# Kernel tuning notes

Measured on AMD Instinct MI355X. Metric: run time of the kernel, lower is better.

The kernel has to match this reference:

```python
import jax, jax.numpy as jnp
import numpy as np

N_BUS = 200000; N_GEN = 50000
E_BB = 1600000; E_GB = 400000; E_BG = 400000
D_IN = 64; H = 32
OUT_BUS = 4; OUT_GEN = 2


def setup_inputs() -> dict:
    key = jax.random.key(0)
    it = iter(jax.random.split(key, 48))
    def nrm(shape, s=0.05):
        return jax.random.normal(next(it), shape, jnp.float32) * s
    inp = {}
    inp["x_bus"] = jax.random.normal(next(it), (N_BUS, D_IN), jnp.float32)
    inp["x_gen"] = jax.random.normal(next(it), (N_GEN, D_IN), jnp.float32)
    inp["src_bb"] = jax.random.randint(next(it), (E_BB,), 0, N_BUS)
    inp["dst_bb"] = jax.random.randint(next(it), (E_BB,), 0, N_BUS)
    inp["src_gb"] = jax.random.randint(next(it), (E_GB,), 0, N_GEN)
    inp["dst_gb"] = jax.random.randint(next(it), (E_GB,), 0, N_BUS)
    inp["src_bg"] = jax.random.randint(next(it), (E_BG,), 0, N_BUS)
    inp["dst_bg"] = jax.random.randint(next(it), (E_BG,), 0, N_GEN)
    # SAGEConv params per layer / relation: lin_l (on aggregated neighbors, with bias),
    # lin_r (root weight on x_dst, no bias) -- matches PyG SAGEConv defaults.
    for lname, din in (("l1", D_IN), ("l2", H)):
        for rel in ("bb", "gb", "bg"):
            inp[f"{lname}_{rel}_Wl"] = nrm((din, H))
            inp[f"{lname}_{rel}_bl"] = jnp.zeros((H,), jnp.float32)
            inp[f"{lname}_{rel}_Wr"] = nrm((din, H))
    for nt, dout in (("bus", OUT_BUS), ("gen", OUT_GEN)):
        inp[f"lin0_{nt}_W"] = nrm((H, H))
        inp[f"lin0_{nt}_b"] = jnp.zeros((H,), jnp.float32)
        inp[f"linf_{nt}_W"] = nrm((H, dout))
        inp[f"linf_{nt}_b"] = jnp.zeros((dout,), jnp.float32)
    return inp


def _sage(x_src, x_dst, src, dst, Wl, bl, Wr, n_dst):
    # SAGEConv: mean-aggregate neighbor features, then out = lin_l(mean) + lin_r(x_dst)
    msg = jax.ops.segment_sum(x_src[src], dst, num_segments=n_dst)
    cnt = jax.ops.segment_sum(jnp.ones((src.shape[0],), x_src.dtype), dst, num_segments=n_dst)
    mean = msg / jnp.maximum(cnt, 1.0)[:, None]
    return mean @ Wl + bl + x_dst @ Wr


def reference(x_bus, x_gen, src_bb, dst_bb, src_gb, dst_gb, src_bg, dst_bg,
              l1_bb_Wl, l1_bb_bl, l1_bb_Wr, l1_gb_Wl, l1_gb_bl, l1_gb_Wr,
              l1_bg_Wl, l1_bg_bl, l1_bg_Wr,
              l2_bb_Wl, l2_bb_bl, l2_bb_Wr, l2_gb_Wl, l2_gb_bl, l2_gb_Wr,
              l2_bg_Wl, l2_bg_bl, l2_bg_Wr,
              lin0_bus_W, lin0_bus_b, lin0_gen_W, lin0_gen_b,
              linf_bus_W, linf_bus_b, linf_gen_W, linf_gen_b):
    # HeteroConv layer 1 (aggr='sum' over relations targeting each dst type)
    hb = (_sage(x_bus, x_bus, src_bb, dst_bb, l1_bb_Wl, l1_bb_bl, l1_bb_Wr, N_BUS)
          + _sage(x_gen, x_bus, src_gb, dst_gb, l1_gb_Wl, l1_gb_bl, l1_gb_Wr, N_BUS))
    hg = _sage(x_bus, x_gen, src_bg, dst_bg, l1_bg_Wl, l1_bg_bl, l1_bg_Wr, N_GEN)
    xb, xg = jax.nn.relu(hb), jax.nn.relu(hg)  # dropout is identity in eval mode
    # HeteroConv layer 2
    hb = (_sage(xb, xb, src_bb, dst_bb, l2_bb_Wl, l2_bb_bl, l2_bb_Wr, N_BUS)
          + _sage(xg, xb, src_gb, dst_gb, l2_gb_Wl, l2_gb_bl, l2_gb_Wr, N_BUS))
    hg = _sage(xb, xg, src_bg, dst_bg, l2_bg_Wl, l2_bg_bl, l2_bg_Wr, N_GEN)
    xb, xg = jax.nn.relu(hb), jax.nn.relu(hg)
    # per-node-type hidden Linear (input relu'd again as in the original; relu is idempotent)
    xb = jax.nn.relu(xb) @ lin0_bus_W + lin0_bus_b
    xg = jax.nn.relu(xg) @ lin0_gen_W + lin0_gen_b
    out_bus = xb @ linf_bus_W + linf_bus_b
    out_gen = xg @ linf_gen_W + linf_gen_b
    return out_bus, out_gen
```

## Files before the change

### kernel.cpp

```cpp
#include <hip/hip_runtime.h>
#include <hip/hip_bf16.h>

#define N_BUS 200000
#define N_GEN 50000
#define E_BB 1600000
#define E_GB 400000
#define E_BG 400000
#define H 32
#define NBINS 1024
#define EPT 16

#define NBK_BUS 782
#define NBK_GEN 196
#define CAP_BB 2560
#define CAP_GB 768
#define CAP_BG 2560

#define NB_PART_BB 391
#define NB_PART_GB 98
#define NB_PART_BG 98
#define NB_PART_ALL 587
#define NB_PREP 32
#define NB_TF_BUS 782
#define NB_TF_GEN 196
#define NB_TF_ALL 978
#define NB_FINE_ALL 1760
#define NB_PL_BUS 6250
#define NB_PL_GEN 1563

#define PNONE 0xFFFFFFFFu

typedef __attribute__((ext_vector_type(8))) short short8;
typedef __attribute__((ext_vector_type(4))) float floatx4;

__device__ inline unsigned short f2bf(float f) {
    __hip_bfloat16 h = __float2bfloat16(f);
    return *reinterpret_cast<unsigned short*>(&h);
}
__device__ inline float bf2f(unsigned short u) {
    return __uint_as_float(((unsigned)u) << 16);
}

__global__ __launch_bounds__(256) void zero_kernel(unsigned* __restrict__ p) {
    int i = blockIdx.x * 256 + threadIdx.x;
    if (i < 3 * NBINS) p[i] = 0u;
}

__device__ __forceinline__ void part_body(int blk, const int* __restrict__ src,
                                          const int* __restrict__ dst, int nE,
                                          unsigned* __restrict__ cnt_g, int CAP,
                                          unsigned* __restrict__ pairs) {
    __shared__ unsigned hist[NBINS];
    __shared__ unsigned base[NBINS];
    __shared__ unsigned sbase[NBINS];
    __shared__ unsigned sh[256];
    __shared__ unsigned pairv[256 * EPT];
    __shared__ unsigned short bid[256 * EPT];
    const int tid = threadIdx.x;
    const int cbase = blk * (256 * EPT);
    const int total = min(256 * EPT, nE - cbase);

    unsigned es[EPT], ed[EPT];
#pragma unroll
    for (int q = 0; q < EPT; q++) {
        int i = cbase + q * 256 + tid;
        if (i < nE) { es[q] = (unsigned)src[i]; ed[q] = (unsigned)dst[i]; }
        else ed[q] = PNONE;
    }
    for (int i = tid; i < NBINS; i += 256) hist[i] = 0;
    __syncthreads();
#pragma unroll
    for (int q = 0; q < EPT; q++)
        if (ed[q] != PNONE) atomicAdd(&hist[ed[q] >> 8], 1u);
    __syncthreads();

    unsigned h4[4];
    unsigned s = 0;
#pragma unroll
    for (int k2 = 0; k2 < 4; k2++) { h4[k2] = hist[tid * 4 + k2]; s += h4[k2]; }
    sh[tid] = s;
    __syncthreads();
#pragma unroll
    for (int d = 1; d < 256; d <<= 1) {
        unsigned t = (tid >= d) ? sh[tid - d] : 0u;
        __syncthreads();
        sh[tid] += t;
        __syncthreads();
    }
    unsigned run = sh[tid] - s;
#pragma unroll
    for (int k2 = 0; k2 < 4; k2++) {
        int b = tid * 4 + k2;
        sbase[b] = run;
        base[b] = h4[k2] ? ((unsigned)b * CAP + atomicAdd(&cnt_g[b], h4[k2])) : 0u;
        hist[b] = 0;
        run += h4[k2];
    }
    __syncthreads();

#pragma unroll
    for (int q = 0; q < EPT; q++) {
        if (ed[q] != PNONE) {
            unsigned b = ed[q] >> 8;
            unsigned off = atomicAdd(&hist[b], 1u);
            unsigned p = sbase[b] + off;
            pairv[p] = ((ed[q] & 255u) << 24) | es[q];
            bid[p] = (unsigned short)b;
        }
    }
    __syncthreads();

    for (int p = tid; p < total; p += 256) {
        unsigned b = bid[p];
        pairs[base[b] + ((unsigned)p - sbase[b])] = pairv[p];
    }
}

__device__ __forceinline__ void prep_body(int pb,
    const float* __restrict__ l1_bb_Wl, const float* __restrict__ l1_bb_bl, const float* __restrict__ l1_bb_Wr,
    const float* __restrict__ l1_gb_Wl, const float* __restrict__ l1_gb_bl, const float* __restrict__ l1_gb_Wr,
    const float* __restrict__ l1_bg_Wl, const float* __restrict__ l1_bg_bl, const float* __restrict__ l1_bg_Wr,
    const float* __restrict__ l2_bb_Wl, const float* __restrict__ l2_bb_bl, const float* __restrict__ l2_bb_Wr,
    const float* __restrict__ l2_gb_Wl, const float* __restrict__ l2_gb_bl, const float* __restrict__ l2_gb_Wr,
    const float* __restrict__ l2_bg_Wl, const float* __restrict__ l2_bg_bl, const float* __restrict__ l2_bg_Wr,
    const float* __restrict__ lin0_bus_W, const float* __restrict__ lin0_bus_b,
    const float* __restrict__ linf_bus_W, const float* __restrict__ linf_bus_b,
    const float* __restrict__ lin0_gen_W, const float* __restrict__ lin0_gen_b,
    const float* __restrict__ linf_gen_W, const float* __restrict__ linf_gen_b,
    unsigned short* __restrict__ Wf1b, float* __restrict__ B1b,
    unsigned short* __restrict__ Wf1g, float* __restrict__ B1g,
    unsigned short* __restrict__ Wf2b, float* __restrict__ B2b,
    unsigned short* __restrict__ Wf2g, float* __restrict__ B2g,
    float* __restrict__ WeB, float* __restrict__ beB,
    float* __restrict__ WeG, float* __restrict__ beG)
{
    int t0 = pb * 256 + threadIdx.x;
    const int NT = NB_PREP * 256;

    for (int f = t0; f < 2 * 6 * 64 * 8; f += NT) {
        int j = f & 7, l = (f >> 3) & 63, tile = f >> 9;
        int nt = tile % 6, kt = tile / 6;
        int k = kt * 32 + (l >> 4) * 8 + j, n = nt * 16 + (l & 15);
        float v;
        if (n < 32) v = l1_bb_Wl[k * 32 + n];
        else if (n < 64) v = l1_bg_Wl[k * 32 + n - 32];
        else v = l1_bb_Wr[k * 32 + n - 64] + l1_gb_Wr[k * 32 + n - 64];
        Wf1b[f] = f2bf(v);
    }
    for (int f = t0; f < 2 * 4 * 64 * 8; f += NT) {
        int j = f & 7, l = (f >> 3) & 63, tile = f >> 9;
        int nt = tile % 4, kt = tile / 4;
        int k = kt * 32 + (l >> 4) * 8 + j, n = nt * 16 + (l & 15);
        float v = (n < 32) ? l1_gb_Wl[k * 32 + n] : l1_bg_Wr[k * 32 + n - 32];
        Wf1g[f] = f2bf(v);
    }
    for (int f = t0; f < 6 * 64 * 8; f += NT) {
        int j = f & 7, l = (f >> 3) & 63, nt = f >> 9;
        int k = (l >> 4) * 8 + j, n = nt * 16 + (l & 15);
        float v;
        if (n < 32) v = l2_bb_Wl[k * 32 + n];
        else if (n < 64) v = l2_bg_Wl[k * 32 + n - 32];
        else v = l2_bb_Wr[k * 32 + n - 64] + l2_gb_Wr[k * 32 + n - 64];
        Wf2b[f] = f2bf(v);
    }
    for (int f = t0; f < 4 * 64 * 8; f += NT) {
        int j = f & 7, l = (f >> 3) & 63, nt = f >> 9;
        int k = (l >> 4) * 8 + j, n = nt * 16 + (l & 15);
        float v = (n < 32) ? l2_gb_Wl[k * 32 + n] : l2_bg_Wr[k * 32 + n - 32];
        Wf2g[f] = f2bf(v);
    }
    if (t0 < 96) {
        B1b[t0] = (t0 < 64) ? 0.0f : l1_bb_bl[t0 - 64] + l1_gb_bl[t0 - 64];
        B2b[t0] = (t0 < 64) ? 0.0f : l2_bb_bl[t0 - 64] + l2_gb_bl[t0 - 64];
    }
    if (t0 < 64) {
        B1g[t0] = (t0 < 32) ? 0.0f : l1_bg_bl[t0 - 32];
        B2g[t0] = (t0 < 32) ? 0.0f : l2_bg_bl[t0 - 32];
    }
    if (t0 < 128) {
        int k = t0 >> 2, c = t0 & 3;
        float s = 0.0f;
        for (int m = 0; m < 32; m++) s += lin0_bus_W[k * 32 + m] * linf_bus_W[m * 4 + c];
        WeB[t0] = s;
    }
    if (t0 >= 128 && t0 < 132) {
        int c = t0 - 128;
        float s = linf_bus_b[c];
        for (int m = 0; m < 32; m++) s += lin0_bus_b[m] * linf_bus_W[m * 4 + c];
        beB[c] = s;
    }
    if (t0 >= 132 && t0 < 196) {
        int i = t0 - 132, k = i >> 1, c = i & 1;
        float s = 0.0f;
        for (int m = 0; m < 32; m++) s += lin0_gen_W[k * 32 + m] * linf_gen_W[m * 2 + c];
        WeG[i] = s;
    }
    if (t0 >= 196 && t0 < 198) {
        int c = t0 - 196;
        float s = linf_gen_b[c];
        for (int m = 0; m < 32; m++) s += lin0_gen_b[m] * linf_gen_W[m * 2 + c];
        beG[c] = s;
    }
}

__global__ __launch_bounds__(256) void prep_part_kernel(
    const int* __restrict__ sbb, const int* __restrict__ dbb, unsigned* __restrict__ cbb, unsigned* __restrict__ pbb,
    const int* __restrict__ sgb, const int* __restrict__ dgb, unsigned* __restrict__ cgb, unsigned* __restrict__ pgb,
    const int* __restrict__ sbg, const int* __restrict__ dbg, unsigned* __restrict__ cbg, unsigned* __restrict__ pbg,
    const float* __restrict__ l1_bb_Wl, const float* __restrict__ l1_bb_bl, const float* __restrict__ l1_bb_Wr,
    const float* __restrict__ l1_gb_Wl, const float* __restrict__ l1_gb_bl, const float* __restrict__ l1_gb_Wr,
    const float* __restrict__ l1_bg_Wl, const float* __restrict__ l1_bg_bl, const float* __restrict__ l1_bg_Wr,
    const float* __restrict__ l2_bb_Wl, const float* __restrict__ l2_bb_bl, const float* __restrict__ l2_bb_Wr,
    const float* __restrict__ l2_gb_Wl, const float* __restrict__ l2_gb_bl, const float* __restrict__ l2_gb_Wr,
    const float* __restrict__ l2_bg_Wl, const float* __restrict__ l2_bg_bl, const float* __restrict__ l2_bg_Wr,
    const float* __restrict__ lin0_bus_W, const float* __restrict__ lin0_bus_b,
    const float* __restrict__ linf_bus_W, const float* __restrict__ linf_bus_b,
    const float* __restrict__ lin0_gen_W, const float* __restrict__ lin0_gen_b,
    const float* __restrict__ linf_gen_W, const float* __restrict__ linf_gen_b,
    unsigned short* __restrict__ Wf1b, float* __restrict__ B1b,
    unsigned short* __restrict__ Wf1g, float* __restrict__ B1g,
    unsigned short* __restrict__ Wf2b, float* __restrict__ B2b,
    unsigned short* __restrict__ Wf2g, float* __restrict__ B2g,
    float* __restrict__ WeB, float* __restrict__ beB,
    float* __restrict__ WeG, float* __restrict__ beG)
{
    int b = blockIdx.x;
    if (b < NB_PART_BB) part_body(b, sbb, dbb, E_BB, cbb, CAP_BB, pbb);
    else if (b < NB_PART_BB + NB_PART_GB) part_body(b - NB_PART_BB, sgb, dgb, E_GB, cgb, CAP_GB, pgb);
    else if (b < NB_PART_ALL) part_body(b - NB_PART_BB - NB_PART_GB, sbg, dbg, E_BG, cbg, CAP_BG, pbg);
    else prep_body(b - NB_PART_ALL,
                   l1_bb_Wl, l1_bb_bl, l1_bb_Wr, l1_gb_Wl, l1_gb_bl, l1_gb_Wr,
                   l1_bg_Wl, l1_bg_bl, l1_bg_Wr, l2_bb_Wl, l2_bb_bl, l2_bb_Wr,
                   l2_gb_Wl, l2_gb_bl, l2_gb_Wr, l2_bg_Wl, l2_bg_bl, l2_bg_Wr,
                   lin0_bus_W, lin0_bus_b, linf_bus_W, linf_bus_b,
                   lin0_gen_W, lin0_gen_b, linf_gen_W, linf_gen_b,
                   Wf1b, B1b, Wf1g, B1g, Wf2b, B2b, Wf2g, B2g, WeB, beB, WeG, beG);
}

__device__ __forceinline__ void fine_body(int b, const unsigned* __restrict__ cnt_g, int CAP,
                                          const unsigned* __restrict__ pairs,
                                          unsigned* __restrict__ rs,
                                          unsigned* __restrict__ esrc, int nDst,
                                          char* __restrict__ lds) {
    unsigned* cnt = (unsigned*)lds;
    unsigned* sh = (unsigned*)(lds + 1024);
    unsigned* stg = (unsigned*)(lds + 2048);
    const int tid = threadIdx.x;
    const unsigned start = (unsigned)b * CAP;
    const unsigned m = cnt_g[b];
    const unsigned end = start + m;

    cnt[tid] = 0;
    __syncthreads();
    for (unsigned k = start + tid; k < end; k += 256)
        atomicAdd(&cnt[pairs[k] >> 24], 1u);
    __syncthreads();
    unsigned c = cnt[tid];
    sh[tid] = c;
    __syncthreads();
#pragma unroll
    for (int d = 1; d < 256; d <<= 1) {
        unsigned t = (tid >= d) ? sh[tid - d] : 0u;
        __syncthreads();
        sh[tid] += t;
        __syncthreads();
    }
    int gd = b * 256 + tid;
    unsigned rowstart = start + sh[tid] - c;
    if (gd < nDst) rs[gd] = (rowstart << 9) | (c < 511u ? c : 511u);
    cnt[tid] = sh[tid] - c;
    __syncthreads();
    for (unsigned k = start + tid; k < end; k += 256) {
        unsigned p = pairs[k];
        unsigned off = atomicAdd(&cnt[p >> 24], 1u);
        stg[off] = p & 0x00FFFFFFu;
    }
    __syncthreads();
    for (unsigned p = tid; p < m; p += 256) esrc[start + p] = stg[p];
}

template <int K, int NOUT, int XS>
__device__ __forceinline__ void mfma_tail(
    int rows, int base,
    const unsigned short* __restrict__ Wf, const float* __restrict__ bias,
    unsigned short* __restrict__ y0, unsigned short* __restrict__ y1, float* __restrict__ h,
    short* lx, float* lo)
{
    constexpr int KT = K / 32, NTN = NOUT / 16, NCH = NOUT / 32;
    constexpr int OS = 34;
    const int tid = threadIdx.x;
    const int w = tid >> 6, l = tid & 63, quad = l >> 4, ln = l & 15;

    short8 bf[KT][NTN];
    const short8* wf8 = (const short8*)Wf;
#pragma unroll
    for (int kt = 0; kt < KT; kt++)
#pragma unroll
        for (int nt = 0; nt < NTN; nt++)
            bf[kt][nt] = wf8[(kt * NTN + nt) * 64 + l];
    float bv[NTN];
#pragma unroll
    for (int nt = 0; nt < NTN; nt++) bv[nt] = bias[nt * 16 + ln];

    floatx4 acc[4][NTN];
#pragma unroll
    for (int mt = 0; mt < 4; mt++)
#pragma unroll
        for (int nt = 0; nt < NTN; nt++) {
            floatx4 c0 = {bv[nt], bv[nt], bv[nt], bv[nt]};
            acc[mt][nt] = c0;
        }
#pragma unroll
    for (int mt = 0; mt < 4; mt++) {
        const int row = w * 64 + mt * 16 + ln;
#pragma unroll
        for (int kt = 0; kt < KT; kt++) {
            short8 af = *(const short8*)&lx[row * XS + kt * 32 + quad * 8];
#pragma unroll
            for (int nt = 0; nt < NTN; nt++)
                acc[mt][nt] = __builtin_amdgcn_mfma_f32_16x16x32_bf16(
                    af, bf[kt][nt], acc[mt][nt], 0, 0, 0);
        }
    }

#pragma unroll
    for (int c = 0; c < NCH; c++) {
        __syncthreads();
#pragma unroll
        for (int mt = 0; mt < 4; mt++)
#pragma unroll
            for (int d = 0; d < 2; d++) {
                int nt = 2 * c + d;
#pragma unroll
                for (int r = 0; r < 4; r++)
                    lo[(w * 64 + mt * 16 + quad * 4 + r) * OS + d * 16 + ln] = acc[mt][nt][r];
            }
        __syncthreads();
        const int T4 = rows * 8;
        if (c == NCH - 1) {
            float* og = h + (size_t)base * 32;
            for (int q = tid; q < T4; q += 256) {
                int r = q >> 3, cc = (q & 7) * 4;
                const float* p = &lo[r * OS + cc];
                *(float4*)(og + q * 4) = make_float4(p[0], p[1], p[2], p[3]);
            }
        } else {
            unsigned short* og = ((c == 0) ? y0 : y1) + (size_t)base * 32;
            for (int q = tid; q < T4; q += 256) {
                int r = q >> 3, cc = (q & 7) * 4;
                const float* p = &lo[r * OS + cc];
                short4 s4;
                s4.x = (short)f2bf(p[0]); s4.y = (short)f2bf(p[1]);
                s4.z = (short)f2bf(p[2]); s4.w = (short)f2bf(p[3]);
                *(short4*)(og + q * 4) = s4;
            }
        }
    }
}

template <int K, int NOUT>
__device__ __forceinline__ void transform_body(
    int blk, const float* x, int n,
    const unsigned short* __restrict__ Wf, const float* __restrict__ bias,
    unsigned short* __restrict__ y0, unsigned short* __restrict__ y1, float* h,
    char* ldsraw)
{
    constexpr int XS = K + 8;
    short* lx = (short*)ldsraw;
    const int tid = threadIdx.x;
    const int base = blk * 256;
    const int rows = min(256, n - base);

    {
        const float4* xg = (const float4*)(x + (size_t)base * K);
        const int T4 = rows * (K / 4);
        for (int q = tid; q < T4; q += 256) {
            float4 v = xg[q];
            int r = q / (K / 4), c = (q % (K / 4)) * 4;
            short4 s4;
            s4.x = (short)f2bf(v.x); s4.y = (short)f2bf(v.y);
            s4.z = (short)f2bf(v.z); s4.w = (short)f2bf(v.w);
            *(short4*)&lx[r * XS + c] = s4;
        }
    }
    __syncthreads();
    mfma_tail<K, NOUT, XS>(rows, base, Wf, bias, y0, y1, h, (short*)ldsraw, (float*)ldsraw);
}

template <int NOUT>
__device__ __forceinline__ void transform_bf16_body(
    int blk, const unsigned short* x, int n,
    const unsigned short* __restrict__ Wf, const float* __restrict__ bias,
    unsigned short* __restrict__ y0, unsigned short* __restrict__ y1, float* h,
    char* ldsraw)
{
    constexpr int K = 32, XS = K + 8;
    short* lx = (short*)ldsraw;
    const int tid = threadIdx.x;
    const int base = blk * 256;
    const int rows = min(256, n - base);

    {
        const short8* xg = (const short8*)(x + (size_t)base * K);
        const int T8 = rows * (K / 8);
        for (int q = tid; q < T8; q += 256) {
            short8 v = xg[q];
            int r = q / (K / 8), c = (q % (K / 8)) * 8;
            *(short8*)&lx[r * XS + c] = v;
        }
    }
    __syncthreads();
    mfma_tail<32, NOUT, XS>(rows, base, Wf, bias, y0, y1, h, (short*)ldsraw, (float*)ldsraw);
}

__global__ __launch_bounds__(256) void tf1_fine_kernel(
    const float* xb, const unsigned short* __restrict__ Wfb, const float* __restrict__ Bb,
    unsigned short* __restrict__ yb0, unsigned short* __restrict__ yb1, float* hb,
    const float* xg, const unsigned short* __restrict__ Wfg, const float* __restrict__ Bg,
    unsigned short* __restrict__ yg0, float* hg,
    const unsigned* __restrict__ cbb, const unsigned* __restrict__ pbb, unsigned* __restrict__ rsbb, unsigned* __restrict__ ebb,
    const unsigned* __restrict__ cgb, const unsigned* __restrict__ pgb, unsigned* __restrict__ rsgb, unsigned* __restrict__ egb,
    const unsigned* __restrict__ cbg, const unsigned* __restrict__ pbg, unsigned* __restrict__ rsbg, unsigned* __restrict__ ebg)
{
    constexpr int XB = 256 * (64 + 8) * 2, OB = 256 * 34 * 4;
    __shared__ __align__(16) char ldsraw[(XB > OB) ? XB : OB];
    int b = blockIdx.x;
    if (b < NB_TF_BUS)
        transform_body<64, 96>(b, xb, N_BUS, Wfb, Bb, yb0, yb1, hb, ldsraw);
    else if (b < NB_TF_ALL)
        transform_body<64, 64>(b - NB_TF_BUS, xg, N_GEN, Wfg, Bg, yg0, nullptr, hg, ldsraw);
    else {
        int f = b - NB_TF_ALL;
        if (f < NBK_BUS) fine_body(f, cbb, CAP_BB, pbb, rsbb, ebb, N_BUS, ldsraw);
        else if (f < 2 * NBK_BUS) fine_body(f - NBK_BUS, cgb, CAP_GB, pgb, rsgb, egb, N_BUS, ldsraw);
        else fine_body(f - 2 * NBK_BUS, cbg, CAP_BG, pbg, rsbg, ebg, N_GEN, ldsraw);
    }
}

__global__ __launch_bounds__(256) void tf2b_all_kernel(
    const unsigned short* x2b, const unsigned short* __restrict__ Wfb, const float* __restrict__ Bb,
    unsigned short* __restrict__ yb0, unsigned short* __restrict__ yb1, float* hb,
    const unsigned short* x2g, const unsigned short* __restrict__ Wfg, const float* __restrict__ Bg,
    unsigned short* __restrict__ yg0, float* hg)
{
    constexpr int XB = 256 * (32 + 8) * 2, OB = 256 * 34 * 4;
    __shared__ __align__(16) char ldsraw[(XB > OB) ? XB : OB];
    int b = blockIdx.x;
    if (b < NB_TF_BUS)
        transform_bf16_body<96>(b, x2b, N_BUS, Wfb, Bb, yb0, yb1, hb, ldsraw);
    else
        transform_bf16_body<64>(b - NB_TF_BUS, x2g, N_GEN, Wfg, Bg, yg0, nullptr, hg, ldsraw);
}

__device__ __forceinline__ void agg_one(
    unsigned u, const unsigned* __restrict__ e,
    const unsigned short* __restrict__ y, int j, float4& r)
{
    unsigned k0 = u >> 9;
    unsigned c = u & 511u;
    unsigned k1 = k0 + c;
    float4 a0 = make_float4(0.f, 0.f, 0.f, 0.f);
    float4 a1 = a0, a2 = a0, a3 = a0;
    unsigned k = k0;
    if (k + 4 <= k1) {
        unsigned s0 = e[k], s1 = e[k + 1], s2 = e[k + 2], s3 = e[k + 3];
        for (; k + 8 <= k1; k += 4) {
            unsigned t0 = e[k + 4], t1 = e[k + 5], t2 = e[k + 6], t3 = e[k + 7];
            ushort4 v0 = *(const ushort4*)(y + (size_t)s0 * H + j);
            ushort4 v1 = *(const ushort4*)(y + (size_t)s1 * H + j);
            ushort4 v2 = *(const ushort4*)(y + (size_t)s2 * H + j);
            ushort4 v3 = *(const ushort4*)(y + (size_t)s3 * H + j);
            a0.x += bf2f(v0.x); a0.y += bf2f(v0.y); a0.z += bf2f(v0.z); a0.w += bf2f(v0.w);
            a1.x += bf2f(v1.x); a1.y += bf2f(v1.y); a1.z += bf2f(v1.z); a1.w += bf2f(v1.w);
            a2.x += bf2f(v2.x); a2.y += bf2f(v2.y); a2.z += bf2f(v2.z); a2.w += bf2f(v2.w);
            a3.x += bf2f(v3.x); a3.y += bf2f(v3.y); a3.z += bf2f(v3.z); a3.w += bf2f(v3.w);
            s0 = t0; s1 = t1; s2 = t2; s3 = t3;
        }
        {
            ushort4 v0 = *(const ushort4*)(y + (size_t)s0 * H + j);
            ushort4 v1 = *(const ushort4*)(y + (size_t)s1 * H + j);
            ushort4 v2 = *(const ushort4*)(y + (size_t)s2 * H + j);
            ushort4 v3 = *(const ushort4*)(y + (size_t)s3 * H + j);
            a0.x += bf2f(v0.x); a0.y += bf2f(v0.y); a0.z += bf2f(v0.z); a0.w += bf2f(v0.w);
            a1.x += bf2f(v1.x); a1.y += bf2f(v1.y); a1.z += bf2f(v1.z); a1.w += bf2f(v1.w);
            a2.x += bf2f(v2.x); a2.y += bf2f(v2.y); a2.z += bf2f(v2.z); a2.w += bf2f(v2.w);
            a3.x += bf2f(v3.x); a3.y += bf2f(v3.y); a3.z += bf2f(v3.z); a3.w += bf2f(v3.w);
            k += 4;
        }
    }
    for (; k < k1; ++k) {
        unsigned s = e[k];
        const ushort4 v = *(const ushort4*)(y + (size_t)s * H + j);
        a0.x += bf2f(v.x); a0.y += bf2f(v.y); a0.z += bf2f(v.z); a0.w += bf2f(v.w);
    }
    a0.x += a1.x + a2.x + a3.x; a0.y += a1.y + a2.y + a3.y;
    a0.z += a1.z + a2.z + a3.z; a0.w += a1.w + a2.w + a3.w;
    float inv = 1.0f / (float)(c > 1u ? c : 1u);
    r.x += a0.x * inv; r.y += a0.y * inv; r.z += a0.z * inv; r.w += a0.w * inv;
}

template <bool FUSE>
__device__ __forceinline__ void pull_body(
    int blk, bool hasB, int n,
    const unsigned* __restrict__ rsA, const unsigned* __restrict__ eA, const unsigned short* __restrict__ yA,
    const unsigned* __restrict__ rsB, const unsigned* __restrict__ eB, const unsigned short* __restrict__ yB,
    const float* __restrict__ h, unsigned short* __restrict__ x2,
    const float* __restrict__ We, const float* __restrict__ be, int DOUT, float* __restrict__ outp)
{
    const int tid = threadIdx.x;
    unsigned node = blk * 32u + (tid >> 3);
    int j = (tid & 7) * 4;
    if (node >= (unsigned)n) return;

    float4 r = *(const float4*)(h + (size_t)node * H + j);

    agg_one(rsA[node], eA, yA, j, r);
    if (hasB) agg_one(rsB[node], eB, yB, j, r);

    if (!FUSE) {
        ushort4 o;
        o.x = f2bf(fmaxf(r.x, 0.f)); o.y = f2bf(fmaxf(r.y, 0.f));
        o.z = f2bf(fmaxf(r.z, 0.f)); o.w = f2bf(fmaxf(r.w, 0.f));
        *(ushort4*)(x2 + (size_t)node * H + j) = o;
        return;
    }

    float p0 = fmaxf(r.x, 0.f), p1 = fmaxf(r.y, 0.f), p2 = fmaxf(r.z, 0.f), p3 = fmaxf(r.w, 0.f);
    float tot[4];
#pragma unroll
    for (int c = 0; c < 4; c++) {
        if (c < DOUT) {
            tot[c] = p0 * We[(j + 0) * DOUT + c] + p1 * We[(j + 1) * DOUT + c]
                   + p2 * We[(j + 2) * DOUT + c] + p3 * We[(j + 3) * DOUT + c];
        } else tot[c] = 0.f;
    }
#pragma unroll
    for (int mask = 1; mask <= 4; mask <<= 1) {
#pragma unroll
        for (int c = 0; c < 4; c++) tot[c] += __shfl_xor(tot[c], mask);
    }
    if ((tid & 7) == 0) {
        if (DOUT == 4) {
            *(float4*)(outp + (size_t)node * 4) =
                make_float4(tot[0] + be[0], tot[1] + be[1], tot[2] + be[2], tot[3] + be[3]);
        } else {
            *(float2*)(outp + (size_t)node * 2) = make_float2(tot[0] + be[0], tot[1] + be[1]);
        }
    }
}

template <bool FUSE>
__global__ __launch_bounds__(256) void pull_all_kernel(
    const unsigned* __restrict__ rsbb, const unsigned* __restrict__ ebb, const unsigned short* __restrict__ ybb,
    const unsigned* __restrict__ rsgb, const unsigned* __restrict__ egb, const unsigned short* __restrict__ ygb,
    const float* __restrict__ hb, unsigned short* __restrict__ x2b,
    const float* __restrict__ WeB, const float* __restrict__ beB,
    const unsigned* __restrict__ rsbg, const unsigned* __restrict__ ebg, const unsigned short* __restrict__ ybg,
    const float* __restrict__ hg, unsigned short* __restrict__ x2g,
    const float* __restrict__ WeG, const float* __restrict__ beG,
    float* __restrict__ outp)
{
    int b = blockIdx.x;
    if (b < NB_PL_BUS)
        pull_body<FUSE>(b, true, N_BUS, rsbb, ebb, ybb, rsgb, egb, ygb, hb, x2b, WeB, beB, 4, outp);
    else
        pull_body<FUSE>(b - NB_PL_BUS, false, N_GEN, rsbg, ebg, ybg, nullptr, nullptr, nullptr,
                        hg, x2g, WeG, beG, 2, outp ? outp + (size_t)N_BUS * 4 : nullptr);
}

extern "C" void kernel_launch(void* const* d_in, const int* in_sizes, int n_in,
                              void* d_out, int out_size, void* d_ws, size_t ws_size,
                              hipStream_t stream) {
    const float* x_bus = (const float*)d_in[0];
    const float* x_gen = (const float*)d_in[1];
    const int* src_bb = (const int*)d_in[2];
    const int* dst_bb = (const int*)d_in[3];
    const int* src_gb = (const int*)d_in[4];
    const int* dst_gb = (const int*)d_in[5];
    const int* src_bg = (const int*)d_in[6];
    const int* dst_bg = (const int*)d_in[7];
    const float* l1_bb_Wl = (const float*)d_in[8];
    const float* l1_bb_bl = (const float*)d_in[9];
    const float* l1_bb_Wr = (const float*)d_in[10];
    const float* l1_gb_Wl = (const float*)d_in[11];
    const float* l1_gb_bl = (const float*)d_in[12];
    const float* l1_gb_Wr = (const float*)d_in[13];
    const float* l1_bg_Wl = (const float*)d_in[14];
    const float* l1_bg_bl = (const float*)d_in[15];
    const float* l1_bg_Wr = (const float*)d_in[16];
    const float* l2_bb_Wl = (const float*)d_in[17];
    const float* l2_bb_bl = (const float*)d_in[18];
    const float* l2_bb_Wr = (const float*)d_in[19];
    const float* l2_gb_Wl = (const float*)d_in[20];
    const float* l2_gb_bl = (const float*)d_in[21];
    const float* l2_gb_Wr = (const float*)d_in[22];
    const float* l2_bg_Wl = (const float*)d_in[23];
    const float* l2_bg_bl = (const float*)d_in[24];
    const float* l2_bg_Wr = (const float*)d_in[25];
    const float* lin0_bus_W = (const float*)d_in[26];
    const float* lin0_bus_b = (const float*)d_in[27];
    const float* linf_bus_W = (const float*)d_in[28];
    const float* linf_bus_b = (const float*)d_in[29];
    const float* lin0_gen_W = (const float*)d_in[30];
    const float* lin0_gen_b = (const float*)d_in[31];
    const float* linf_gen_W = (const float*)d_in[32];
    const float* linf_gen_b = (const float*)d_in[33];

    char* ws = (char*)d_ws;
    size_t off = 0;
    auto alloc = [&](size_t bytes) {
        char* p = ws + off;
        off += (bytes + 255) & ~(size_t)255;
        return p;
    };
    unsigned* rs_bb = (unsigned*)alloc((size_t)N_BUS * 4);
    unsigned* rs_gb = (unsigned*)alloc((size_t)N_BUS * 4);
    unsigned* rs_bg = (unsigned*)alloc((size_t)N_GEN * 4);
    unsigned* cur_bb = (unsigned*)alloc(NBINS * 4);
    unsigned* cur_gb = (unsigned*)alloc(NBINS * 4);
    unsigned* cur_bg = (unsigned*)alloc(NBINS * 4);
    unsigned* e_bb = (unsigned*)alloc((size_t)NBK_BUS * CAP_BB * 4);
    unsigned* e_gb = (unsigned*)alloc((size_t)NBK_BUS * CAP_GB * 4);
    unsigned* e_bg = (unsigned*)alloc((size_t)NBK_GEN * CAP_BG * 4);
    unsigned* p_bb = (unsigned*)alloc((size_t)NBK_BUS * CAP_BB * 4);
    unsigned* p_gb = (unsigned*)alloc((size_t)NBK_BUS * CAP_GB * 4);
    unsigned* p_bg = (unsigned*)alloc((size_t)NBK_GEN * CAP_BG * 4);
    unsigned short* y_bb = (unsigned short*)alloc((size_t)N_BUS * H * 2);
    unsigned short* y_bg = (unsigned short*)alloc((size_t)N_BUS * H * 2);
    unsigned short* y_gb = (unsigned short*)alloc((size_t)N_GEN * H * 2);
    float* h_bus = (float*)alloc((size_t)N_BUS * H * 4);
    float* h_gen = (float*)alloc((size_t)N_GEN * H * 4);
    unsigned short* x2_bus = (unsigned short*)alloc((size_t)N_BUS * H * 2);
    unsigned short* x2_gen = (unsigned short*)alloc((size_t)N_GEN * H * 2);
    unsigned short* Wf1b = (unsigned short*)alloc(2 * 6 * 64 * 8 * 2);
    float* B1b = (float*)alloc(96 * 4);
    unsigned short* Wf1g = (unsigned short*)alloc(2 * 4 * 64 * 8 * 2);
    float* B1g = (float*)alloc(64 * 4);
    unsigned short* Wf2b = (unsigned short*)alloc(6 * 64 * 8 * 2);
    float* B2b = (float*)alloc(96 * 4);
    unsigned short* Wf2g = (unsigned short*)alloc(4 * 64 * 8 * 2);
    float* B2g = (float*)alloc(64 * 4);
    float* WeB = (float*)alloc(128 * 4);
    float* beB = (float*)alloc(4 * 4);
    float* WeG = (float*)alloc(64 * 4);
    float* beG = (float*)alloc(2 * 4);

    zero_kernel<<<12, 256, 0, stream>>>(cur_bb);

    prep_part_kernel<<<NB_PART_ALL + NB_PREP, 256, 0, stream>>>(
        src_bb, dst_bb, cur_bb, p_bb, src_gb, dst_gb, cur_gb, p_gb,
        src_bg, dst_bg, cur_bg, p_bg,
        l1_bb_Wl, l1_bb_bl, l1_bb_Wr, l1_gb_Wl, l1_gb_bl, l1_gb_Wr,
        l1_bg_Wl, l1_bg_bl, l1_bg_Wr, l2_bb_Wl, l2_bb_bl, l2_bb_Wr,
        l2_gb_Wl, l2_gb_bl, l2_gb_Wr, l2_bg_Wl, l2_bg_bl, l2_bg_Wr,
        lin0_bus_W, lin0_bus_b, linf_bus_W, linf_bus_b,
        lin0_gen_W, lin0_gen_b, linf_gen_W, linf_gen_b,
        Wf1b, B1b, Wf1g, B1g, Wf2b, B2b, Wf2g, B2g, WeB, beB, WeG, beG);

    tf1_fine_kernel<<<NB_TF_ALL + NB_FINE_ALL, 256, 0, stream>>>(
        x_bus, Wf1b, B1b, y_bb, y_bg, h_bus, x_gen, Wf1g, B1g, y_gb, h_gen,
        cur_bb, p_bb, rs_bb, e_bb, cur_gb, p_gb, rs_gb, e_gb, cur_bg, p_bg, rs_bg, e_bg);

    pull_all_kernel<false><<<NB_PL_BUS + NB_PL_GEN, 256, 0, stream>>>(
        rs_bb, e_bb, y_bb, rs_gb, e_gb, y_gb, h_bus, x2_bus, WeB, beB,
        rs_bg, e_bg, y_bg, h_gen, x2_gen, WeG, beG, nullptr);

    tf2b_all_kernel<<<NB_TF_BUS + NB_TF_GEN, 256, 0, stream>>>(
        x2_bus, Wf2b, B2b, y_bb, y_bg, h_bus, x2_gen, Wf2g, B2g, y_gb, h_gen);

    pull_all_kernel<true><<<NB_PL_BUS + NB_PL_GEN, 256, 0, stream>>>(
        rs_bb, e_bb, y_bb, rs_gb, e_gb, y_gb, h_bus, nullptr, WeB, beB,
        rs_bg, e_bg, y_bg, h_gen, nullptr, WeG, beG, (float*)d_out);
}
```

Measured before the change: 354.3 us.

## Fuse layer-1 aggregation with layer-2 MFMA transform into one kernel

Merges the first pull/aggregate kernel and the layer-2 transform kernel. Each 32-node block now aggregates neighbours, applies relu, stages the bf16 activations in LDS and runs the MFMA transform in place. This drops the x2 intermediate round trip through global memory and one kernel launch. Because the new kernel reads the layer-1 y buffers while producing layer-2 outputs, separate y2 buffers are needed. Each block now does small 32-row MFMA tiles with extra syncthreads, which may lower transform efficiency.

```diff
diff --git a/kernel.cpp b/kernel.cpp
--- a/kernel.cpp
+++ b/kernel.cpp
@@ -387,32 +387,6 @@
     mfma_tail<K, NOUT, XS>(rows, base, Wf, bias, y0, y1, h, (short*)ldsraw, (float*)ldsraw);
 }
 
-template <int NOUT>
-__device__ __forceinline__ void transform_bf16_body(
-    int blk, const unsigned short* x, int n,
-    const unsigned short* __restrict__ Wf, const float* __restrict__ bias,
-    unsigned short* __restrict__ y0, unsigned short* __restrict__ y1, float* h,
-    char* ldsraw)
-{
-    constexpr int K = 32, XS = K + 8;
-    short* lx = (short*)ldsraw;
-    const int tid = threadIdx.x;
-    const int base = blk * 256;
-    const int rows = min(256, n - base);
-
-    {
-        const short8* xg = (const short8*)(x + (size_t)base * K);
-        const int T8 = rows * (K / 8);
-        for (int q = tid; q < T8; q += 256) {
-            short8 v = xg[q];
-            int r = q / (K / 8), c = (q % (K / 8)) * 8;
-            *(short8*)&lx[r * XS + c] = v;
-        }
-    }
-    __syncthreads();
-    mfma_tail<32, NOUT, XS>(rows, base, Wf, bias, y0, y1, h, (short*)ldsraw, (float*)ldsraw);
-}
-
 __global__ __launch_bounds__(256) void tf1_fine_kernel(
     const float* xb, const unsigned short* __restrict__ Wfb, const float* __restrict__ Bb,
     unsigned short* __restrict__ yb0, unsigned short* __restrict__ yb1, float* hb,
@@ -435,21 +409,6 @@
         else if (f < 2 * NBK_BUS) fine_body(f - NBK_BUS, cgb, CAP_GB, pgb, rsgb, egb, N_BUS, ldsraw);
         else fine_body(f - 2 * NBK_BUS, cbg, CAP_BG, pbg, rsbg, ebg, N_GEN, ldsraw);
     }
-}
-
-__global__ __launch_bounds__(256) void tf2b_all_kernel(
-    const unsigned short* x2b, const unsigned short* __restrict__ Wfb, const float* __restrict__ Bb,
-    unsigned short* __restrict__ yb0, unsigned short* __restrict__ yb1, float* hb,
-    const unsigned short* x2g, const unsigned short* __restrict__ Wfg, const float* __restrict__ Bg,
-    unsigned short* __restrict__ yg0, float* hg)
-{
-    constexpr int XB = 256 * (32 + 8) * 2, OB = 256 * 34 * 4;
-    __shared__ __align__(16) char ldsraw[(XB > OB) ? XB : OB];
-    int b = blockIdx.x;
-    if (b < NB_TF_BUS)
-        transform_bf16_body<96>(b, x2b, N_BUS, Wfb, Bb, yb0, yb1, hb, ldsraw);
-    else
-        transform_bf16_body<64>(b - NB_TF_BUS, x2g, N_GEN, Wfg, Bg, yg0, nullptr, hg, ldsraw);
 }
 
 __device__ __forceinline__ void agg_one(
@@ -499,12 +458,103 @@
     r.x += a0.x * inv; r.y += a0.y * inv; r.z += a0.z * inv; r.w += a0.w * inv;
 }
 
-template <bool FUSE>
-__device__ __forceinline__ void pull_body(
+template <int NTA, bool HASB>
+__device__ __forceinline__ void pull_tf_body(
+    int blk, int n,
+    const unsigned* __restrict__ rsA, const unsigned* __restrict__ eA, const unsigned short* __restrict__ yA,
+    const unsigned* __restrict__ rsB, const unsigned* __restrict__ eB, const unsigned short* __restrict__ yB,
+    float* __restrict__ h,
+    const unsigned short* __restrict__ Wf, const float* __restrict__ bias,
+    unsigned short* __restrict__ z0, unsigned short* __restrict__ z1,
+    short* __restrict__ lx, float* __restrict__ lo)
+{
+    constexpr int XS = 40;
+    constexpr int OS = 34;
+    const int tid = threadIdx.x;
+    const int row = tid >> 3;
+    const int j = (tid & 7) * 4;
+    const int base = blk * 32;
+    const int node = base + row;
+    const bool act = node < n;
+
+    float4 r = make_float4(0.f, 0.f, 0.f, 0.f);
+    if (act) {
+        r = *(const float4*)(h + (size_t)node * H + j);
+        agg_one(rsA[node], eA, yA, j, r);
+        if (HASB) agg_one(rsB[node], eB, yB, j, r);
+    }
+    short4 s4;
+    s4.x = (short)f2bf(fmaxf(r.x, 0.f));
+    s4.y = (short)f2bf(fmaxf(r.y, 0.f));
+    s4.z = (short)f2bf(fmaxf(r.z, 0.f));
+    s4.w = (short)f2bf(fmaxf(r.w, 0.f));
+    *(short4*)&lx[row * XS + j] = s4;
+    __syncthreads();
+
+    const int w = tid >> 6, l = tid & 63, quad = l >> 4, ln = l & 15;
+    const int mt = w & 1, ngrp = w >> 1;
+    const short8* wf8 = (const short8*)Wf;
+    floatx4 acc[NTA];
+    short8 af = *(const short8*)&lx[(mt * 16 + ln) * XS + quad * 8];
+#pragma unroll
+    for (int i = 0; i < NTA; i++) {
+        int nt = 2 * i + ngrp;
+        float bv = bias[nt * 16 + ln];
+        floatx4 c0 = {bv, bv, bv, bv};
+        acc[i] = __builtin_amdgcn_mfma_f32_16x16x32_bf16(af, wf8[nt * 64 + l], c0, 0, 0, 0);
+    }
+
+    const int rows = min(32, n - base);
+    const int orow = tid >> 3, oc = (tid & 7) * 4;
+#pragma unroll
+    for (int c = 0; c < NTA; c++) {
+        __syncthreads();
+#pragma unroll
+        for (int rr = 0; rr < 4; rr++)
+            lo[(mt * 16 + quad * 4 + rr) * OS + ngrp * 16 + ln] = acc[c][rr];
+        __syncthreads();
+        if (orow < rows) {
+            const float* p = &lo[orow * OS + oc];
+            if (c == NTA - 1) {
+                *(float4*)(h + (size_t)(base + orow) * H + oc) =
+                    make_float4(p[0], p[1], p[2], p[3]);
+            } else {
+                unsigned short* og = (c == 0) ? z0 : z1;
+                short4 o;
+                o.x = (short)f2bf(p[0]); o.y = (short)f2bf(p[1]);
+                o.z = (short)f2bf(p[2]); o.w = (short)f2bf(p[3]);
+                *(short4*)(og + (size_t)(base + orow) * H + oc) = o;
+            }
+        }
+    }
+}
+
+__global__ __launch_bounds__(256) void pull_tf2_kernel(
+    const unsigned* __restrict__ rsbb, const unsigned* __restrict__ ebb, const unsigned short* __restrict__ ybb,
+    const unsigned* __restrict__ rsgb, const unsigned* __restrict__ egb, const unsigned short* __restrict__ ygb,
+    float* __restrict__ hb, const unsigned short* __restrict__ Wfb, const float* __restrict__ Bb,
+    unsigned short* __restrict__ y2bb, unsigned short* __restrict__ y2bg,
+    const unsigned* __restrict__ rsbg, const unsigned* __restrict__ ebg, const unsigned short* __restrict__ ybg,
+    float* __restrict__ hg, const unsigned short* __restrict__ Wfg, const float* __restrict__ Bg,
+    unsigned short* __restrict__ y2gb)
+{
+    __shared__ __align__(16) short lx[32 * 40];
+    __shared__ __align__(16) float lo[32 * 34];
+    int b = blockIdx.x;
+    if (b < NB_PL_BUS)
+        pull_tf_body<3, true>(b, N_BUS, rsbb, ebb, ybb, rsgb, egb, ygb,
+                              hb, Wfb, Bb, y2bb, y2bg, lx, lo);
+    else
+        pull_tf_body<2, false>(b - NB_PL_BUS, N_GEN, rsbg, ebg, ybg,
+                               nullptr, nullptr, nullptr,
+                               hg, Wfg, Bg, y2gb, nullptr, lx, lo);
+}
+
+__device__ __forceinline__ void pull_head_body(
     int blk, bool hasB, int n,
     const unsigned* __restrict__ rsA, const unsigned* __restrict__ eA, const unsigned short* __restrict__ yA,
     const unsigned* __restrict__ rsB, const unsigned* __restrict__ eB, const unsigned short* __restrict__ yB,
-    const float* __restrict__ h, unsigned short* __restrict__ x2,
+    const float* __restrict__ h,
     const float* __restrict__ We, const float* __restrict__ be, int DOUT, float* __restrict__ outp)
 {
     const int tid = threadIdx.x;
@@ -516,14 +566,6 @@
 
     agg_one(rsA[node], eA, yA, j, r);
     if (hasB) agg_one(rsB[node], eB, yB, j, r);
-
-    if (!FUSE) {
-        ushort4 o;
-        o.x = f2bf(fmaxf(r.x, 0.f)); o.y = f2bf(fmaxf(r.y, 0.f));
-        o.z = f2bf(fmaxf(r.z, 0.f)); o.w = f2bf(fmaxf(r.w, 0.f));
-        *(ushort4*)(x2 + (size_t)node * H + j) = o;
-        return;
-    }
 
     float p0 = fmaxf(r.x, 0.f), p1 = fmaxf(r.y, 0.f), p2 = fmaxf(r.z, 0.f), p3 = fmaxf(r.w, 0.f);
     float tot[4];
@@ -549,23 +591,20 @@
     }
 }
 
-template <bool FUSE>
-__global__ __launch_bounds__(256) void pull_all_kernel(
-    const unsigned* __restrict__ rsbb, const unsigned* __restrict__ ebb, const unsigned short* __restrict__ ybb,
-    const unsigned* __restrict__ rsgb, const unsigned* __restrict__ egb, const unsigned short* __restrict__ ygb,
-    const float* __restrict__ hb, unsigned short* __restrict__ x2b,
-    const float* __restrict__ WeB, const float* __restrict__ beB,
-    const unsigned* __restrict__ rsbg, const unsigned* __restrict__ ebg, const unsigned short* __restrict__ ybg,
-    const float* __restrict__ hg, unsigned short* __restrict__ x2g,
-    const float* __restrict__ WeG, const float* __restrict__ beG,
+__global__ __launch_bounds__(256) void pull_head_kernel(
+    const unsigned* __restrict__ rsbb, const unsigned* __restrict__ ebb, const unsigned short* __restrict__ y2bb,
+    const unsigned* __restrict__ rsgb, const unsigned* __restrict__ egb, const unsigned short* __restrict__ y2gb,
+    const float* __restrict__ hb, const float* __restrict__ WeB, const float* __restrict__ beB,
+    const unsigned* __restrict__ rsbg, const unsigned* __restrict__ ebg, const unsigned short* __restrict__ y2bg,
+    const float* __restrict__ hg, const float* __restrict__ WeG, const float* __restrict__ beG,
     float* __restrict__ outp)
 {
     int b = blockIdx.x;
     if (b < NB_PL_BUS)
-        pull_body<FUSE>(b, true, N_BUS, rsbb, ebb, ybb, rsgb, egb, ygb, hb, x2b, WeB, beB, 4, outp);
+        pull_head_body(b, true, N_BUS, rsbb, ebb, y2bb, rsgb, egb, y2gb, hb, WeB, beB, 4, outp);
     else
-        pull_body<FUSE>(b - NB_PL_BUS, false, N_GEN, rsbg, ebg, ybg, nullptr, nullptr, nullptr,
-                        hg, x2g, WeG, beG, 2, outp ? outp + (size_t)N_BUS * 4 : nullptr);
+        pull_head_body(b - NB_PL_BUS, false, N_GEN, rsbg, ebg, y2bg, nullptr, nullptr, nullptr,
+                       hg, WeG, beG, 2, outp + (size_t)N_BUS * 4);
 }
 
 extern "C" void kernel_launch(void* const* d_in, const int* in_sizes, int n_in,
@@ -628,10 +667,11 @@
     unsigned short* y_bb = (unsigned short*)alloc((size_t)N_BUS * H * 2);
     unsigned short* y_bg = (unsigned short*)alloc((size_t)N_BUS * H * 2);
     unsigned short* y_gb = (unsigned short*)alloc((size_t)N_GEN * H * 2);
+    unsigned short* y2_bb = (unsigned short*)alloc((size_t)N_BUS * H * 2);
+    unsigned short* y2_bg = (unsigned short*)alloc((size_t)N_BUS * H * 2);
+    unsigned short* y2_gb = (unsigned short*)alloc((size_t)N_GEN * H * 2);
     float* h_bus = (float*)alloc((size_t)N_BUS * H * 4);
     float* h_gen = (float*)alloc((size_t)N_GEN * H * 4);
-    unsigned short* x2_bus = (unsigned short*)alloc((size_t)N_BUS * H * 2);
-    unsigned short* x2_gen = (unsigned short*)alloc((size_t)N_GEN * H * 2);
     unsigned short* Wf1b = (unsigned short*)alloc(2 * 6 * 64 * 8 * 2);
     float* B1b = (float*)alloc(96 * 4);
     unsigned short* Wf1g = (unsigned short*)alloc(2 * 4 * 64 * 8 * 2);
@@ -661,14 +701,11 @@
         x_bus, Wf1b, B1b, y_bb, y_bg, h_bus, x_gen, Wf1g, B1g, y_gb, h_gen,
         cur_bb, p_bb, rs_bb, e_bb, cur_gb, p_gb, rs_gb, e_gb, cur_bg, p_bg, rs_bg, e_bg);
 
-    pull_all_kernel<false><<<NB_PL_BUS + NB_PL_GEN, 256, 0, stream>>>(
-        rs_bb, e_bb, y_bb, rs_gb, e_gb, y_gb, h_bus, x2_bus, WeB, beB,
-        rs_bg, e_bg, y_bg, h_gen, x2_gen, WeG, beG, nullptr);
-
-    tf2b_all_kernel<<<NB_TF_BUS + NB_TF_GEN, 256, 0, stream>>>(
-        x2_bus, Wf2b, B2b, y_bb, y_bg, h_bus, x2_gen, Wf2g, B2g, y_gb, h_gen);
-
-    pull_all_kernel<true><<<NB_PL_BUS + NB_PL_GEN, 256, 0, stream>>>(
-        rs_bb, e_bb, y_bb, rs_gb, e_gb, y_gb, h_bus, nullptr, WeB, beB,
-        rs_bg, e_bg, y_bg, h_gen, nullptr, WeG, beG, (float*)d_out);
-}
+    pull_tf2_kernel<<<NB_PL_BUS + NB_PL_GEN, 256, 0, stream>>>(
+        rs_bb, e_bb, y_bb, rs_gb, e_gb, y_gb, h_bus, Wf2b, B2b, y2_bb, y2_bg,
+        rs_bg, e_bg, y_bg, h_gen, Wf2g, B2g, y2_gb);
+
+    pull_head_kernel<<<NB_PL_BUS + NB_PL_GEN, 256, 0, stream>>>(
+        rs_bb, e_bb, y2_bb, rs_gb, e_gb, y2_gb, h_bus, WeB, beB,
+        rs_bg, e_bg, y2_bg, h_gen, WeG, beG, (float*)d_out);
+}
```

Measured after the change: 359.2 us. No clear change (+1.4%).
